# Performance work log

Measured on AMD Instinct MI355X. Metric: run time of the kernel, lower is better.

The kernel has to match this reference:

```python
import jax, jax.numpy as jnp
import numpy as np

B, S, D = 4, 4096, 1024
H, HKV, DH = 16, 4, 64
C = 256            # chunk_size
HALF_W = 128       # sliding_window // 2 (attend iff |i-j| <= HALF_W)
EPS = 1e-6


def _rope_tables(seq_len, dh):
    inv_freq = 1.0 / (10000.0 ** (np.arange(0, dh, 2, dtype=np.float32) / dh))
    t = np.arange(seq_len, dtype=np.float32)
    ang = np.einsum('s,f->sf', t, inv_freq)          # [S, dh/2]
    emb = np.concatenate([ang, ang], axis=-1)        # [S, dh]
    return jnp.asarray(np.cos(emb)), jnp.asarray(np.sin(emb))


def setup_inputs() -> dict:
    key = jax.random.key(0)
    ks = jax.random.split(key, 6)
    w = 0.02
    cos, sin = _rope_tables(S, DH)
    return {
        'x':  jax.random.normal(ks[0], (B, S, D), dtype=jnp.float32),
        'Wq': jax.random.normal(ks[1], (D, H * DH), dtype=jnp.float32) * w,
        'bq': jnp.zeros((H * DH,), jnp.float32),
        'Wk': jax.random.normal(ks[2], (D, HKV * DH), dtype=jnp.float32) * w,
        'bk': jnp.zeros((HKV * DH,), jnp.float32),
        'Wv': jax.random.normal(ks[3], (D, HKV * DH), dtype=jnp.float32) * w,
        'bv': jnp.zeros((HKV * DH,), jnp.float32),
        'Wo': jax.random.normal(ks[4], (H * DH, D), dtype=jnp.float32) * w,
        'bo': jnp.zeros((D,), jnp.float32),
        'qn_w': jnp.ones((DH,), jnp.float32),
        'kn_w': jnp.ones((DH,), jnp.float32),
        'cos': cos,
        'sin': sin,
    }


def _rmsnorm(t, w):
    var = jnp.mean(t * t, axis=-1, keepdims=True)
    return t * jax.lax.rsqrt(var + EPS) * w


def _rotate_half(t):
    t1, t2 = jnp.split(t, 2, axis=-1)
    return jnp.concatenate([-t2, t1], axis=-1)


def _apply_rope(t, cos, sin):
    # t: [B, h, S, dh]; cos/sin: [S, dh]
    return t * cos[None, None] + _rotate_half(t) * sin[None, None]


def _neighbor_blocks(t, nc):
    # t: [B, h, S, dh] -> [B, h, nc, 3C, dh] (prev, cur, next chunk; zero-padded ends)
    tp = jnp.pad(t, ((0, 0), (0, 0), (C, C), (0, 0)))
    tp = tp.reshape(t.shape[0], t.shape[1], nc + 2, C, t.shape[-1])
    return jnp.concatenate([tp[:, :, :-2], tp[:, :, 1:-1], tp[:, :, 2:]], axis=3)


def forward(x, Wq, bq, Wk, bk, Wv, bv, Wo, bo, qn_w, kn_w, cos, sin):
    b, s, _ = x.shape
    nc = s // C
    q = (x @ Wq + bq).reshape(b, s, H, DH).transpose(0, 2, 1, 3)     # [B,H,S,dh]
    k = (x @ Wk + bk).reshape(b, s, HKV, DH).transpose(0, 2, 1, 3)   # [B,Hkv,S,dh]
    v = (x @ Wv + bv).reshape(b, s, HKV, DH).transpose(0, 2, 1, 3)
    q = _rmsnorm(q, qn_w)
    k = _rmsnorm(k, kn_w)
    q = _apply_rope(q, cos, sin)
    k = _apply_rope(k, cos, sin)
    # GQA: repeat kv heads
    rep = H // HKV
    k = jnp.repeat(k, rep, axis=1)
    v = jnp.repeat(v, rep, axis=1)

    qc = q.reshape(b, H, nc, C, DH)
    kb = _neighbor_blocks(k, nc)   # [B,H,nc,3C,dh]
    vb = _neighbor_blocks(v, nc)

    scale = 1.0 / np.sqrt(DH).astype(np.float32)
    scores = jnp.einsum('bhncd,bhnkd->bhnck', qc, kb) * scale        # [B,H,nc,C,3C]

    iq = jnp.arange(C)[:, None]                  # query pos within chunk
    jk = jnp.arange(3 * C)[None, :]              # key pos within block
    rel = jk - C - iq                            # key_global - query_global
    c_idx = jnp.arange(nc)[:, None, None]
    gkj = (c_idx - 1) * C + jk[None]             # global key index [nc,C,3C]
    mask = (jnp.abs(rel)[None] <= HALF_W) & (gkj >= 0) & (gkj < s)
    scores = jnp.where(mask[None, None], scores, jnp.float32(-1e30))
    attn = jax.nn.softmax(scores, axis=-1)
    out = jnp.einsum('bhnck,bhnkd->bhncd', attn, vb)                 # [B,H,nc,C,dh]
    out = out.reshape(b, H, s, DH).transpose(0, 2, 1, 3).reshape(b, s, H * DH)
    return out @ Wo + bo


def reference(x, Wq, bq, Wk, bk, Wv, bv, Wo, bo, qn_w, kn_w, cos, sin):
    return forward(x, Wq, bq, Wk, bk, Wv, bv, Wo, bo, qn_w, kn_w, cos, sin)
```

## Files before the change

kernel.cpp:

```cpp
#include <hip/hip_runtime.h>
#include <stdint.h>

typedef __bf16 bf16_t;
typedef __bf16 bf16x8 __attribute__((ext_vector_type(8)));
typedef __bf16 bf16x4 __attribute__((ext_vector_type(4)));
typedef float  f32x4  __attribute__((ext_vector_type(4)));

#define MFMA_BF16(a,b,c) __builtin_amdgcn_mfma_f32_16x16x32_bf16((a),(b),(c),0,0,0)

constexpr int kB = 4;
constexpr int kS = 4096;
constexpr int kD = 1024;
constexpr int kH = 16;
constexpr int kHKV = 4;
constexpr int kDH = 64;
constexpr int kChunk = 256;

__global__ __launch_bounds__(256) void k_cvt_bf16(const float* __restrict__ in,
                                                  bf16_t* __restrict__ out, int n4){
  int i = blockIdx.x * 256 + threadIdx.x;
  if (i >= n4) return;
  float4 v = ((const float4*)in)[i];
  bf16x4 o;
  o[0] = (__bf16)v.x; o[1] = (__bf16)v.y; o[2] = (__bf16)v.z; o[3] = (__bf16)v.w;
  ((bf16x4*)out)[i] = o;
}

__global__ __launch_bounds__(256) void k_transpose_cvt(const float* __restrict__ W,
                                                       bf16_t* __restrict__ Wt,
                                                       int K, int N){
  __shared__ float t[32][33];
  int n0 = blockIdx.x * 32, k0 = blockIdx.y * 32;
  int tx = threadIdx.x & 31, ty = threadIdx.x >> 5;
#pragma unroll
  for (int i = 0; i < 4; i++){
    int kkk = ty + i*8;
    t[kkk][tx] = W[(size_t)(k0+kkk)*N + n0 + tx];
  }
  __syncthreads();
#pragma unroll
  for (int i = 0; i < 4; i++){
    int nn = ty + i*8;
    Wt[(size_t)(n0+nn)*K + k0 + tx] = (__bf16)t[tx][nn];
  }
}

template<bool BF16OUT>
__global__ __launch_bounds__(256) void k_gemm_bt(const bf16_t* __restrict__ A,
                                                 const bf16_t* __restrict__ Bt,
                                                 const float* __restrict__ bias,
                                                 void* __restrict__ outp,
                                                 int M, int N, int K){
  (void)M;
  __shared__ bf16_t Al[128][72];
  __shared__ bf16_t Bl[128][72];
  const int tid = threadIdx.x;
  const int lane = tid & 63;
  const int wave = tid >> 6;
  const int wm = wave >> 1, wn = wave & 1;
  const int bm = blockIdx.y, bn = blockIdx.x;
  const int l15 = lane & 15, l4 = lane >> 4;
  f32x4 acc[4][4];
#pragma unroll
  for (int a = 0; a < 4; a++)
#pragma unroll
    for (int b = 0; b < 4; b++)
#pragma unroll
      for (int r = 0; r < 4; r++) acc[a][b][r] = 0.f;

  for (int kt = 0; kt < K; kt += 64){
    __syncthreads();
#pragma unroll
    for (int i = 0; i < 4; i++){
      int task = i*256 + tid;
      int rr = task >> 3, c8 = task & 7;
      *(bf16x8*)&Al[rr][c8*8] = *(const bf16x8*)(A + (size_t)(bm*128 + rr)*K + kt + c8*8);
      *(bf16x8*)&Bl[rr][c8*8] = *(const bf16x8*)(Bt + (size_t)(bn*128 + rr)*K + kt + c8*8);
    }
    __syncthreads();
#pragma unroll
    for (int ks = 0; ks < 2; ks++){
      bf16x8 af[4], bfr[4];
#pragma unroll
      for (int mt = 0; mt < 4; mt++) af[mt]  = *(const bf16x8*)&Al[wm*64 + mt*16 + l15][ks*32 + l4*8];
#pragma unroll
      for (int nt = 0; nt < 4; nt++) bfr[nt] = *(const bf16x8*)&Bl[wn*64 + nt*16 + l15][ks*32 + l4*8];
#pragma unroll
      for (int mt = 0; mt < 4; mt++)
#pragma unroll
        for (int nt = 0; nt < 4; nt++)
          acc[mt][nt] = MFMA_BF16(af[mt], bfr[nt], acc[mt][nt]);
    }
  }
#pragma unroll
  for (int mt = 0; mt < 4; mt++){
#pragma unroll
    for (int nt = 0; nt < 4; nt++){
      int row0 = bm*128 + wm*64 + mt*16 + l4*4;
      int col  = bn*128 + wn*64 + nt*16 + l15;
      float bv = bias[col];
#pragma unroll
      for (int r = 0; r < 4; r++){
        float v = acc[mt][nt][r] + bv;
        if (BF16OUT) ((bf16_t*)outp)[(size_t)(row0 + r)*N + col] = (__bf16)v;
        else         ((float*)outp)[(size_t)(row0 + r)*N + col] = v;
      }
    }
  }
}

__global__ __launch_bounds__(256) void k_norm_rope(const float* __restrict__ qin,
                                                   const float* __restrict__ kin,
                                                   const float* __restrict__ qw,
                                                   const float* __restrict__ kw,
                                                   const float* __restrict__ cosb,
                                                   const float* __restrict__ sinb,
                                                   bf16_t* __restrict__ qout,
                                                   bf16_t* __restrict__ kout){
  const int g = blockIdx.x * 16 + (threadIdx.x >> 4);
  const int ln = threadIdx.x & 15;
  const int NQ = (kB*kS) * kH;
  const float* src; bf16_t* dst; const float* w;
  int row;
  if (g < NQ){
    row = g >> 4; int head = g & 15;
    src = qin + (size_t)row*1024 + head*64;
    dst = qout + (size_t)row*1024 + head*64;
    w = qw;
  } else {
    int gk = g - NQ;
    row = gk >> 2; int head = gk & 3;
    src = kin + (size_t)row*256 + head*64;
    dst = kout + (size_t)row*256 + head*64;
    w = kw;
  }
  float t0 = src[ln], t1 = src[ln+16], t2 = src[ln+32], t3 = src[ln+48];
  float ss = t0*t0 + t1*t1 + t2*t2 + t3*t3;
  ss += __shfl_xor(ss, 1); ss += __shfl_xor(ss, 2);
  ss += __shfl_xor(ss, 4); ss += __shfl_xor(ss, 8);
  float rs = rsqrtf(ss * (1.0f/64.0f) + 1e-6f);
  t0 *= rs * w[ln];    t1 *= rs * w[ln+16];
  t2 *= rs * w[ln+32]; t3 *= rs * w[ln+48];
  int s = row & (kS - 1);
  const float* cp = cosb + (size_t)s*64;
  const float* sp = sinb + (size_t)s*64;
  float o0 = t0*cp[ln]    - t2*sp[ln];
  float o1 = t1*cp[ln+16] - t3*sp[ln+16];
  float o2 = t2*cp[ln+32] + t0*sp[ln+32];
  float o3 = t3*cp[ln+48] + t1*sp[ln+48];
  dst[ln]    = (__bf16)o0; dst[ln+16] = (__bf16)o1;
  dst[ln+32] = (__bf16)o2; dst[ln+48] = (__bf16)o3;
}

__global__ __launch_bounds__(256) void k_attn(const bf16_t* __restrict__ q,
                                              const bf16_t* __restrict__ kbuf,
                                              const bf16_t* __restrict__ vbuf,
                                              bf16_t* __restrict__ o){
  __shared__ bf16_t Kl[64][72];
  __shared__ bf16_t Vt[64][72];
  __shared__ bf16_t Pl[4][64][72];
  const int c = blockIdx.x, h = blockIdx.y, b = blockIdx.z;
  const int hkv = h >> 2;
  const int tid = threadIdx.x;
  const int lane = tid & 63, w = tid >> 6;
  const int l15 = lane & 15, l4 = lane >> 4;
  const int qrow0 = c*kChunk + w*64;

  bf16x8 qf[4][2];
#pragma unroll
  for (int mt = 0; mt < 4; mt++)
#pragma unroll
    for (int ks = 0; ks < 2; ks++)
      qf[mt][ks] = *(const bf16x8*)(q + (size_t)(b*kS + qrow0 + mt*16 + l15)*1024
                                      + h*64 + ks*32 + l4*8);

  f32x4 acc[4][4];
  float m_run[4][4], l_run[4][4];
#pragma unroll
  for (int mt = 0; mt < 4; mt++){
#pragma unroll
    for (int dt = 0; dt < 4; dt++)
#pragma unroll
      for (int r = 0; r < 4; r++) acc[mt][dt][r] = 0.f;
#pragma unroll
    for (int r = 0; r < 4; r++){ m_run[mt][r] = -1e30f; l_run[mt][r] = 0.f; }
  }

  for (int kt = 0; kt < 8; kt++){
    const int kg0 = c*kChunk - 128 + kt*64;
    __syncthreads();
#pragma unroll
    for (int it = 0; it < 2; it++){
      int task = it*256 + tid;
      int key = task >> 3, c8 = task & 7;
      int kg = kg0 + key;
      bf16x8 kv8, vv8;
      if (kg >= 0 && kg < kS){
        size_t base = (size_t)(b*kS + kg)*256 + hkv*64 + c8*8;
        kv8 = *(const bf16x8*)(kbuf + base);
        vv8 = *(const bf16x8*)(vbuf + base);
      } else {
#pragma unroll
        for (int e = 0; e < 8; e++){ kv8[e] = (__bf16)0.f; vv8[e] = (__bf16)0.f; }
      }
      *(bf16x8*)&Kl[key][c8*8] = kv8;
#pragma unroll
      for (int e = 0; e < 8; e++) Vt[c8*8 + e][key] = vv8[e];
    }
    __syncthreads();

    bf16x8 kf[4][2];
#pragma unroll
    for (int nt = 0; nt < 4; nt++)
#pragma unroll
      for (int ks = 0; ks < 2; ks++)
        kf[nt][ks] = *(const bf16x8*)&Kl[nt*16 + l15][ks*32 + l4*8];

#pragma unroll
    for (int mt = 0; mt < 4; mt++){
      f32x4 sc[4];
#pragma unroll
      for (int nt = 0; nt < 4; nt++)
#pragma unroll
        for (int r = 0; r < 4; r++) sc[nt][r] = 0.f;
#pragma unroll
      for (int ks = 0; ks < 2; ks++)
#pragma unroll
        for (int nt = 0; nt < 4; nt++)
          sc[nt] = MFMA_BF16(qf[mt][ks], kf[nt][ks], sc[nt]);

      const int qg0 = qrow0 + mt*16 + l4*4;
#pragma unroll
      for (int nt = 0; nt < 4; nt++){
        int kg = kg0 + nt*16 + l15;
        bool kgok = (kg >= 0) && (kg < kS);
#pragma unroll
        for (int r = 0; r < 4; r++){
          int rel = kg - (qg0 + r);
          bool okm = kgok && (rel >= -128) && (rel <= 128);
          sc[nt][r] = okm ? sc[nt][r]*0.125f : -1e30f;
        }
      }
      float mx[4], fct[4], rsum[4];
#pragma unroll
      for (int r = 0; r < 4; r++){
        mx[r] = fmaxf(fmaxf(sc[0][r], sc[1][r]), fmaxf(sc[2][r], sc[3][r]));
        mx[r] = fmaxf(mx[r], __shfl_xor(mx[r], 1));
        mx[r] = fmaxf(mx[r], __shfl_xor(mx[r], 2));
        mx[r] = fmaxf(mx[r], __shfl_xor(mx[r], 4));
        mx[r] = fmaxf(mx[r], __shfl_xor(mx[r], 8));
        float mn = fmaxf(m_run[mt][r], mx[r]);
        fct[r] = __expf(m_run[mt][r] - mn);
        m_run[mt][r] = mn;
        rsum[r] = 0.f;
      }
#pragma unroll
      for (int nt = 0; nt < 4; nt++)
#pragma unroll
        for (int r = 0; r < 4; r++){
          float p = __expf(sc[nt][r] - m_run[mt][r]);
          rsum[r] += p;
          sc[nt][r] = p;
        }
#pragma unroll
      for (int r = 0; r < 4; r++){
        rsum[r] += __shfl_xor(rsum[r], 1);
        rsum[r] += __shfl_xor(rsum[r], 2);
        rsum[r] += __shfl_xor(rsum[r], 4);
        rsum[r] += __shfl_xor(rsum[r], 8);
        l_run[mt][r] = l_run[mt][r]*fct[r] + rsum[r];
      }
#pragma unroll
      for (int dt = 0; dt < 4; dt++)
#pragma unroll
        for (int r = 0; r < 4; r++) acc[mt][dt][r] *= fct[r];
#pragma unroll
      for (int nt = 0; nt < 4; nt++)
#pragma unroll
        for (int r = 0; r < 4; r++)
          Pl[w][mt*16 + l4*4 + r][nt*16 + l15] = (__bf16)sc[nt][r];
    }

    bf16x8 vf[2][4];
#pragma unroll
    for (int ks = 0; ks < 2; ks++)
#pragma unroll
      for (int dt = 0; dt < 4; dt++)
        vf[ks][dt] = *(const bf16x8*)&Vt[dt*16 + l15][ks*32 + l4*8];
#pragma unroll
    for (int mt = 0; mt < 4; mt++)
#pragma unroll
      for (int ks = 0; ks < 2; ks++){
        bf16x8 pf = *(const bf16x8*)&Pl[w][mt*16 + l15][ks*32 + l4*8];
#pragma unroll
        for (int dt = 0; dt < 4; dt++)
          acc[mt][dt] = MFMA_BF16(pf, vf[ks][dt], acc[mt][dt]);
      }
  }

#pragma unroll
  for (int mt = 0; mt < 4; mt++)
#pragma unroll
    for (int dt = 0; dt < 4; dt++){
      int row = b*kS + qrow0 + mt*16 + l4*4;
      int col = h*64 + dt*16 + l15;
#pragma unroll
      for (int r = 0; r < 4; r++){
        float ov = acc[mt][dt][r] / l_run[mt][r];
        o[(size_t)(row + r)*1024 + col] = (__bf16)ov;
      }
    }
}

extern "C" void kernel_launch(void* const* d_in, const int* in_sizes, int n_in,
                              void* d_out, int out_size, void* d_ws, size_t ws_size,
                              hipStream_t stream){
  (void)in_sizes; (void)n_in; (void)out_size; (void)ws_size;
  const float* x    = (const float*)d_in[0];
  const float* Wq   = (const float*)d_in[1];
  const float* bq   = (const float*)d_in[2];
  const float* Wk   = (const float*)d_in[3];
  const float* bk   = (const float*)d_in[4];
  const float* Wv   = (const float*)d_in[5];
  const float* bv   = (const float*)d_in[6];
  const float* Wo   = (const float*)d_in[7];
  const float* bo   = (const float*)d_in[8];
  const float* qn_w = (const float*)d_in[9];
  const float* kn_w = (const float*)d_in[10];
  const float* cosb = (const float*)d_in[11];
  const float* sinb = (const float*)d_in[12];
  float* out = (float*)d_out;

  char* ws = (char*)d_ws;
  const size_t MB = 1024ull*1024ull;
  bf16_t* x_b  = (bf16_t*)(ws);
  bf16_t* q_b  = (bf16_t*)(ws + 32*MB);
  bf16_t* k_b  = (bf16_t*)(ws + 64*MB);
  bf16_t* v_b  = (bf16_t*)(ws + 72*MB);
  float*  k_f  = (float*) (ws + 80*MB);
  bf16_t* wq_t = (bf16_t*)(ws + 96*MB);
  bf16_t* wo_t = (bf16_t*)(ws + 98*MB);
  bf16_t* wk_t = (bf16_t*)(ws + 100*MB);
  bf16_t* wv_t = (bf16_t*)(ws + 100*MB + 512*1024);
  bf16_t* attn_b = x_b;
  float*  q_f  = out;

  k_cvt_bf16<<<dim3(16384), dim3(256), 0, stream>>>(x, x_b, (kB*kS*kD)/4);
  k_transpose_cvt<<<dim3(32, 32), dim3(256), 0, stream>>>(Wq, wq_t, 1024, 1024);
  k_transpose_cvt<<<dim3(8, 32),  dim3(256), 0, stream>>>(Wk, wk_t, 1024, 256);
  k_transpose_cvt<<<dim3(8, 32),  dim3(256), 0, stream>>>(Wv, wv_t, 1024, 256);
  k_transpose_cvt<<<dim3(32, 32), dim3(256), 0, stream>>>(Wo, wo_t, 1024, 1024);

  k_gemm_bt<false><<<dim3(8, 128), dim3(256), 0, stream>>>(x_b, wq_t, bq, (void*)q_f, 16384, 1024, 1024);
  k_gemm_bt<false><<<dim3(2, 128), dim3(256), 0, stream>>>(x_b, wk_t, bk, (void*)k_f, 16384, 256, 1024);
  k_gemm_bt<true ><<<dim3(2, 128), dim3(256), 0, stream>>>(x_b, wv_t, bv, (void*)v_b, 16384, 256, 1024);

  k_norm_rope<<<dim3(20480), dim3(256), 0, stream>>>(q_f, k_f, qn_w, kn_w, cosb, sinb, q_b, k_b);

  k_attn<<<dim3(16, 16, 4), dim3(256), 0, stream>>>(q_b, k_b, v_b, attn_b);

  k_gemm_bt<false><<<dim3(8, 128), dim3(256), 0, stream>>>(attn_b, wo_t, bo, (void*)out, 16384, 1024, 1024);
}
```

Before: 488.5 us.

## Use direct global-to-LDS swizzled loads in GEMM and skip masked attention tiles

```diff
diff --git a/kernel.cpp b/kernel.cpp
--- a/kernel.cpp
+++ b/kernel.cpp
@@ -15,6 +15,11 @@
 constexpr int kHKV = 4;
 constexpr int kDH = 64;
 constexpr int kChunk = 256;
+
+__device__ __forceinline__ void gload_lds16(const bf16_t* g, bf16_t* l){
+  __builtin_amdgcn_global_load_lds((const __attribute__((address_space(1))) void*)g,
+                                   (__attribute__((address_space(3))) void*)l, 16, 0, 0);
+}
 
 __global__ __launch_bounds__(256) void k_cvt_bf16(const float* __restrict__ in,
                                                   bf16_t* __restrict__ out, int n4){
@@ -52,14 +57,17 @@
                                                  void* __restrict__ outp,
                                                  int M, int N, int K){
   (void)M;
-  __shared__ bf16_t Al[128][72];
-  __shared__ bf16_t Bl[128][72];
+  __shared__ bf16_t Al[128*64];
+  __shared__ bf16_t Bl[128*64];
   const int tid = threadIdx.x;
   const int lane = tid & 63;
   const int wave = tid >> 6;
   const int wm = wave >> 1, wn = wave & 1;
   const int bm = blockIdx.y, bn = blockIdx.x;
   const int l15 = lane & 15, l4 = lane >> 4;
+  const int s_row = lane >> 3;
+  const int s_bc  = lane & 7;
+  const int s_colE = (s_bc ^ s_row) * 8;
   f32x4 acc[4][4];
 #pragma unroll
   for (int a = 0; a < 4; a++)
@@ -72,19 +80,24 @@
     __syncthreads();
 #pragma unroll
     for (int i = 0; i < 4; i++){
-      int task = i*256 + tid;
-      int rr = task >> 3, c8 = task & 7;
-      *(bf16x8*)&Al[rr][c8*8] = *(const bf16x8*)(A + (size_t)(bm*128 + rr)*K + kt + c8*8);
-      *(bf16x8*)&Bl[rr][c8*8] = *(const bf16x8*)(Bt + (size_t)(bn*128 + rr)*K + kt + c8*8);
+      int rowA = (wave*4 + i)*8 + s_row;
+      gload_lds16(A  + (size_t)(bm*128 + rowA)*K + kt + s_colE, &Al[(wave*4 + i)*512]);
+      gload_lds16(Bt + (size_t)(bn*128 + rowA)*K + kt + s_colE, &Bl[(wave*4 + i)*512]);
     }
     __syncthreads();
 #pragma unroll
     for (int ks = 0; ks < 2; ks++){
       bf16x8 af[4], bfr[4];
 #pragma unroll
-      for (int mt = 0; mt < 4; mt++) af[mt]  = *(const bf16x8*)&Al[wm*64 + mt*16 + l15][ks*32 + l4*8];
-#pragma unroll
-      for (int nt = 0; nt < 4; nt++) bfr[nt] = *(const bf16x8*)&Bl[wn*64 + nt*16 + l15][ks*32 + l4*8];
+      for (int mt = 0; mt < 4; mt++){
+        int row = wm*64 + mt*16 + l15;
+        af[mt] = *(const bf16x8*)&Al[(row*64 + ks*32 + l4*8) ^ ((row & 7)*8)];
+      }
+#pragma unroll
+      for (int nt = 0; nt < 4; nt++){
+        int row = wn*64 + nt*16 + l15;
+        bfr[nt] = *(const bf16x8*)&Bl[(row*64 + ks*32 + l4*8) ^ ((row & 7)*8)];
+      }
 #pragma unroll
       for (int mt = 0; mt < 4; mt++)
 #pragma unroll
@@ -156,7 +169,6 @@
                                               const bf16_t* __restrict__ kbuf,
                                               const bf16_t* __restrict__ vbuf,
                                               bf16_t* __restrict__ o){
-  __shared__ bf16_t Kl[64][72];
   __shared__ bf16_t Vt[64][72];
   __shared__ bf16_t Pl[4][64][72];
   const int c = blockIdx.x, h = blockIdx.y, b = blockIdx.z;
@@ -188,114 +200,127 @@
 
   for (int kt = 0; kt < 8; kt++){
     const int kg0 = c*kChunk - 128 + kt*64;
+    const bool active = (kt >= w) && (kt <= w + 4);
     __syncthreads();
-#pragma unroll
-    for (int it = 0; it < 2; it++){
-      int task = it*256 + tid;
-      int key = task >> 3, c8 = task & 7;
-      int kg = kg0 + key;
-      bf16x8 kv8, vv8;
-      if (kg >= 0 && kg < kS){
-        size_t base = (size_t)(b*kS + kg)*256 + hkv*64 + c8*8;
-        kv8 = *(const bf16x8*)(kbuf + base);
-        vv8 = *(const bf16x8*)(vbuf + base);
-      } else {
-#pragma unroll
-        for (int e = 0; e < 8; e++){ kv8[e] = (__bf16)0.f; vv8[e] = (__bf16)0.f; }
-      }
-      *(bf16x8*)&Kl[key][c8*8] = kv8;
-#pragma unroll
-      for (int e = 0; e < 8; e++) Vt[c8*8 + e][key] = vv8[e];
-    }
-    __syncthreads();
 
     bf16x8 kf[4][2];
-#pragma unroll
-    for (int nt = 0; nt < 4; nt++)
-#pragma unroll
-      for (int ks = 0; ks < 2; ks++)
-        kf[nt][ks] = *(const bf16x8*)&Kl[nt*16 + l15][ks*32 + l4*8];
-
-#pragma unroll
-    for (int mt = 0; mt < 4; mt++){
-      f32x4 sc[4];
-#pragma unroll
-      for (int nt = 0; nt < 4; nt++)
-#pragma unroll
-        for (int r = 0; r < 4; r++) sc[nt][r] = 0.f;
-#pragma unroll
-      for (int ks = 0; ks < 2; ks++)
-#pragma unroll
-        for (int nt = 0; nt < 4; nt++)
-          sc[nt] = MFMA_BF16(qf[mt][ks], kf[nt][ks], sc[nt]);
-
-      const int qg0 = qrow0 + mt*16 + l4*4;
+    if (active){
 #pragma unroll
       for (int nt = 0; nt < 4; nt++){
         int kg = kg0 + nt*16 + l15;
-        bool kgok = (kg >= 0) && (kg < kS);
+        if (kg >= 0 && kg < kS){
+          const bf16_t* kr = kbuf + (size_t)(b*kS + kg)*256 + hkv*64;
+#pragma unroll
+          for (int ks = 0; ks < 2; ks++)
+            kf[nt][ks] = *(const bf16x8*)(kr + ks*32 + l4*8);
+        } else {
+#pragma unroll
+          for (int ks = 0; ks < 2; ks++)
+#pragma unroll
+            for (int e = 0; e < 8; e++) kf[nt][ks][e] = (__bf16)0.f;
+        }
+      }
+    }
+
+#pragma unroll
+    for (int it = 0; it < 2; it++){
+      int key = tid & 63;
+      int c8  = (tid >> 6) + it*4;
+      int kg = kg0 + key;
+      bf16x8 vv8;
+      if (kg >= 0 && kg < kS){
+        vv8 = *(const bf16x8*)(vbuf + (size_t)(b*kS + kg)*256 + hkv*64 + c8*8);
+      } else {
+#pragma unroll
+        for (int e = 0; e < 8; e++) vv8[e] = (__bf16)0.f;
+      }
+#pragma unroll
+      for (int e = 0; e < 8; e++) Vt[c8*8 + e][key] = vv8[e];
+    }
+    __syncthreads();
+
+    if (active){
+#pragma unroll
+      for (int mt = 0; mt < 4; mt++){
+        f32x4 sc[4];
+#pragma unroll
+        for (int nt = 0; nt < 4; nt++)
+#pragma unroll
+          for (int r = 0; r < 4; r++) sc[nt][r] = 0.f;
+#pragma unroll
+        for (int ks = 0; ks < 2; ks++)
+#pragma unroll
+          for (int nt = 0; nt < 4; nt++)
+            sc[nt] = MFMA_BF16(qf[mt][ks], kf[nt][ks], sc[nt]);
+
+        const int qg0 = qrow0 + mt*16 + l4*4;
+#pragma unroll
+        for (int nt = 0; nt < 4; nt++){
+          int kg = kg0 + nt*16 + l15;
+          bool kgok = (kg >= 0) && (kg < kS);
+#pragma unroll
+          for (int r = 0; r < 4; r++){
+            int rel = kg - (qg0 + r);
+            bool okm = kgok && (rel >= -128) && (rel <= 128);
+            sc[nt][r] = okm ? sc[nt][r]*0.125f : -1e30f;
+          }
+        }
+        float mx[4], fct[4], rsum[4];
 #pragma unroll
         for (int r = 0; r < 4; r++){
-          int rel = kg - (qg0 + r);
-          bool okm = kgok && (rel >= -128) && (rel <= 128);
-          sc[nt][r] = okm ? sc[nt][r]*0.125f : -1e30f;
-        }
-      }
-      float mx[4], fct[4], rsum[4];
-#pragma unroll
-      for (int r = 0; r < 4; r++){
-        mx[r] = fmaxf(fmaxf(sc[0][r], sc[1][r]), fmaxf(sc[2][r], sc[3][r]));
-        mx[r] = fmaxf(mx[r], __shfl_xor(mx[r], 1));
-        mx[r] = fmaxf(mx[r], __shfl_xor(mx[r], 2));
-        mx[r] = fmaxf(mx[r], __shfl_xor(mx[r], 4));
-        mx[r] = fmaxf(mx[r], __shfl_xor(mx[r], 8));
-        float mn = fmaxf(m_run[mt][r], mx[r]);
-        fct[r] = __expf(m_run[mt][r] - mn);
-        m_run[mt][r] = mn;
-        rsum[r] = 0.f;
-      }
-#pragma unroll
-      for (int nt = 0; nt < 4; nt++)
+          mx[r] = fmaxf(fmaxf(sc[0][r], sc[1][r]), fmaxf(sc[2][r], sc[3][r]));
+          mx[r] = fmaxf(mx[r], __shfl_xor(mx[r], 1));
+          mx[r] = fmaxf(mx[r], __shfl_xor(mx[r], 2));
+          mx[r] = fmaxf(mx[r], __shfl_xor(mx[r], 4));
+          mx[r] = fmaxf(mx[r], __shfl_xor(mx[r], 8));
+          float mn = fmaxf(m_run[mt][r], mx[r]);
+          fct[r] = __expf(m_run[mt][r] - mn);
+          m_run[mt][r] = mn;
+          rsum[r] = 0.f;
+        }
+#pragma unroll
+        for (int nt = 0; nt < 4; nt++)
+#pragma unroll
+          for (int r = 0; r < 4; r++){
+            float p = __expf(sc[nt][r] - m_run[mt][r]);
+            rsum[r] += p;
+            sc[nt][r] = p;
+          }
 #pragma unroll
         for (int r = 0; r < 4; r++){
-          float p = __expf(sc[nt][r] - m_run[mt][r]);
-          rsum[r] += p;
-          sc[nt][r] = p;
-        }
-#pragma unroll
-      for (int r = 0; r < 4; r++){
-        rsum[r] += __shfl_xor(rsum[r], 1);
-        rsum[r] += __shfl_xor(rsum[r], 2);
-        rsum[r] += __shfl_xor(rsum[r], 4);
-        rsum[r] += __shfl_xor(rsum[r], 8);
-        l_run[mt][r] = l_run[mt][r]*fct[r] + rsum[r];
-      }
-#pragma unroll
-      for (int dt = 0; dt < 4; dt++)
-#pragma unroll
-        for (int r = 0; r < 4; r++) acc[mt][dt][r] *= fct[r];
-#pragma unroll
-      for (int nt = 0; nt < 4; nt++)
-#pragma unroll
-        for (int r = 0; r < 4; r++)
-          Pl[w][mt*16 + l4*4 + r][nt*16 + l15] = (__bf16)sc[nt][r];
-    }
-
-    bf16x8 vf[2][4];
-#pragma unroll
-    for (int ks = 0; ks < 2; ks++)
-#pragma unroll
-      for (int dt = 0; dt < 4; dt++)
-        vf[ks][dt] = *(const bf16x8*)&Vt[dt*16 + l15][ks*32 + l4*8];
-#pragma unroll
-    for (int mt = 0; mt < 4; mt++)
-#pragma unroll
-      for (int ks = 0; ks < 2; ks++){
-        bf16x8 pf = *(const bf16x8*)&Pl[w][mt*16 + l15][ks*32 + l4*8];
+          rsum[r] += __shfl_xor(rsum[r], 1);
+          rsum[r] += __shfl_xor(rsum[r], 2);
+          rsum[r] += __shfl_xor(rsum[r], 4);
+          rsum[r] += __shfl_xor(rsum[r], 8);
+          l_run[mt][r] = l_run[mt][r]*fct[r] + rsum[r];
+        }
 #pragma unroll
         for (int dt = 0; dt < 4; dt++)
-          acc[mt][dt] = MFMA_BF16(pf, vf[ks][dt], acc[mt][dt]);
-      }
+#pragma unroll
+          for (int r = 0; r < 4; r++) acc[mt][dt][r] *= fct[r];
+#pragma unroll
+        for (int nt = 0; nt < 4; nt++)
+#pragma unroll
+          for (int r = 0; r < 4; r++)
+            Pl[w][mt*16 + l4*4 + r][nt*16 + l15] = (__bf16)sc[nt][r];
+      }
+
+      bf16x8 vf[2][4];
+#pragma unroll
+      for (int ks = 0; ks < 2; ks++)
+#pragma unroll
+        for (int dt = 0; dt < 4; dt++)
+          vf[ks][dt] = *(const bf16x8*)&Vt[dt*16 + l15][ks*32 + l4*8];
+#pragma unroll
+      for (int mt = 0; mt < 4; mt++)
+#pragma unroll
+        for (int ks = 0; ks < 2; ks++){
+          bf16x8 pf = *(const bf16x8*)&Pl[w][mt*16 + l15][ks*32 + l4*8];
+#pragma unroll
+          for (int dt = 0; dt < 4; dt++)
+            acc[mt][dt] = MFMA_BF16(pf, vf[ks][dt], acc[mt][dt]);
+        }
+    }
   }
 
 #pragma unroll
```

Result: slower. 504.3 us (+3.2%).
